# Optimization experiments

Measured on AMD Instinct MI355X. Metric: run time of the kernel, lower is better.

The kernel has to match this reference:

```python
import jax, jax.numpy as jnp
import numpy as np

B, N, D = 16, 1024, 16  # graphs, nodes, embedding_dim


def setup_inputs() -> dict:
    key = jax.random.key(0)
    ks = jax.random.split(key, 13)
    s = 0.05  # small weight scale to keep exp(alpha) well-behaved
    return {
        "X": jax.random.normal(ks[0], (B, N, D), dtype=jnp.float32),
        "init_param": jax.random.normal(ks[1], (2,), dtype=jnp.float32) * s,
        "Wq": jax.random.normal(ks[2], (D - 1, D, D), dtype=jnp.float32) * s,
        "bq": jax.random.normal(ks[3], (D - 1, D), dtype=jnp.float32) * s,
        "Wk": jax.random.normal(ks[4], (D - 1, D, D), dtype=jnp.float32) * s,
        "bk": jax.random.normal(ks[5], (D - 1, D), dtype=jnp.float32) * s,
        "Wv": jax.random.normal(ks[6], (D - 1, D, D), dtype=jnp.float32) * s,
        "bv": jax.random.normal(ks[7], (D - 1, D), dtype=jnp.float32) * s,
        "Wo": jax.random.normal(ks[8], (D - 1, D, D), dtype=jnp.float32) * s,
        "bo": jax.random.normal(ks[9], (D - 1, D), dtype=jnp.float32) * s,
        "Wf": jax.random.normal(ks[10], (D - 1, 2, D), dtype=jnp.float32) * s,
        "bf": jax.random.normal(ks[11], (D - 1, 2), dtype=jnp.float32) * s,
    }


def reference(X, init_param, Wq, bq, Wk, bk, Wv, bv, Wo, bo, Wf, bf):
    b, n, d = X.shape
    dt = X.dtype
    Zs = []
    logdet = jnp.zeros((b, n), dt)
    for i in range(d):
        if i == 0:
            mu, alpha = init_param[0], init_param[1]
        else:
            l = i - 1
            Xi = X[:, :, :i]  # [B,N,i] growing ragged slice
            Q = Xi @ Wq[l, :i, :i].T + bq[l, :i]
            K = Xi @ Wk[l, :i, :i].T + bk[l, :i]
            V = Xi @ Wv[l, :i, :i].T + bv[l, :i]
            # SAB/MAB: softmax(QK^T / sqrt(dim_V=i)); num_heads=1
            A = jax.nn.softmax(
                jnp.einsum("bnd,bmd->bnm", Q, K) / jnp.sqrt(jnp.asarray(i, dt)),
                axis=-1,
            )  # [B,N,N]
            O = Q + jnp.einsum("bnm,bmd->bnd", A, V)
            O = O + jax.nn.relu(O @ Wo[l, :i, :i].T + bo[l, :i])
            out = O @ Wf[l, :, :i].T + bf[l]  # [B,N,2]
            mu, alpha = out[..., 0], out[..., 1]
        Zs.append((X[:, :, i] - mu) / jnp.exp(alpha))
        logdet = logdet - alpha
    Z = jnp.stack(Zs, axis=-1)
    return Z, logdet
```

## Files before the change

kernel.cpp:

```cpp
#include <hip/hip_runtime.h>
#include <math.h>

#define Bb 16
#define Nn 1024
#define Dd 16
#define NL 15

typedef __attribute__((ext_vector_type(8))) short short8;
typedef __attribute__((ext_vector_type(16))) float f32x16;
typedef __attribute__((ext_vector_type(4))) unsigned uint4v;

#if __has_builtin(__builtin_amdgcn_exp2f)
#define EXP2(x) __builtin_amdgcn_exp2f(x)
#else
#define EXP2(x) exp2f(x)
#endif

#define VSTR 1040
#define V_OFF 32768
#define ONES_OFF 66048
#define RS_OFF 69632
#define LDS_TOTAL 73728

__device__ __forceinline__ unsigned pack2bf(float a, float b) {
    unsigned ua = __float_as_uint(a) + 0x8000u;
    unsigned ub = __float_as_uint(b) + 0x8000u;
    return (ua >> 16) | (ub & 0xffff0000u);
}
__device__ __forceinline__ unsigned short bf1(float a) {
    return (unsigned short)((__float_as_uint(a) + 0x8000u) >> 16);
}

__device__ __forceinline__ unsigned expperm(float x, float y) {
    unsigned ex = __float_as_uint(EXP2(x));
    unsigned ey = __float_as_uint(EXP2(y));
#if __has_builtin(__builtin_amdgcn_perm)
    return __builtin_amdgcn_perm(ey, ex, 0x07060302);
#else
    return (ex >> 16) | (ey & 0xffff0000u);
#endif
}

__device__ __forceinline__ int vperm(int m) {
    return (m & 3) + ((m & 8) >> 1) + ((m & 4) << 1);
}

__device__ __forceinline__ void project(const float* __restrict__ xrow,
                                        const float* __restrict__ W,
                                        const float* __restrict__ bias,
                                        int i, float* __restrict__ q) {
#pragma unroll
    for (int r = 0; r < 16; r++) q[r] = 0.f;
    for (int c = 0; c < i; c++) {
        float xc = xrow[c];
#pragma unroll
        for (int r = 0; r < 16; r++) q[r] = fmaf(xc, W[r * 16 + c], q[r]);
    }
#pragma unroll
    for (int r = 0; r < 16; r++) q[r] = (r < i) ? (q[r] + bias[r]) : 0.f;
}

__device__ __forceinline__ void load_row16(const float* __restrict__ p, float* __restrict__ x) {
    const float4* xp = (const float4*)p;
    float4 a = xp[0], b = xp[1], c = xp[2], d = xp[3];
    x[0]=a.x; x[1]=a.y; x[2]=a.z; x[3]=a.w;
    x[4]=b.x; x[5]=b.y; x[6]=b.z; x[7]=b.w;
    x[8]=c.x; x[9]=c.y; x[10]=c.z; x[11]=c.w;
    x[12]=d.x; x[13]=d.y; x[14]=d.z; x[15]=d.w;
}

__global__ void gf_init(const float* __restrict__ X, const float* __restrict__ ip,
                        float* __restrict__ out) {
    int idx = blockIdx.x * blockDim.x + threadIdx.x;
    if (idx >= Bb * Nn) return;
    float mu = ip[0], alpha = ip[1];
    float x0 = X[(size_t)idx * Dd];
    out[(size_t)idx * Dd] = (x0 - mu) * __expf(-alpha);
    out[(size_t)Bb * Nn * Dd + idx] = -alpha;
}

__launch_bounds__(1024, 4)
__global__ void gf_fused(const float* __restrict__ X,
                         const float* __restrict__ Wq, const float* __restrict__ bq,
                         const float* __restrict__ Wk, const float* __restrict__ bk,
                         const float* __restrict__ Wv, const float* __restrict__ bv,
                         const float* __restrict__ Wo, const float* __restrict__ bo,
                         const float* __restrict__ Wf, const float* __restrict__ bf,
                         float* __restrict__ out) {
    extern __shared__ char smem[];
    const int l = blockIdx.x, b = blockIdx.y, i = l + 1;
    const int t = threadIdx.x;
    const int wid = t >> 6, lane = t & 63;
    const int q31 = lane & 31, h = lane >> 5;
    const float qscale = 1.4426950408889634f * rsqrtf((float)i);

    unsigned short* Ksh  = (unsigned short*)smem;
    unsigned short* Vsh  = (unsigned short*)(smem + V_OFF);
    unsigned short* Ones = (unsigned short*)(smem + ONES_OFF);

    const float* Xb  = X  + (size_t)b * Nn * Dd;
    const float* wq  = Wq + l * 256;  const float* bql = bq + l * 16;
    const float* wk  = Wk + l * 256;  const float* bkl = bk + l * 16;
    const float* wvp = Wv + l * 256;  const float* bvl = bv + l * 16;
    const float* wo  = Wo + l * 256;  const float* bol = bo + l * 16;
    const float* wf  = Wf + l * 32;   const float* bfl = bf + l * 2;

    unsigned qu[8];
    {
        float xr[16]; load_row16(Xb + (size_t)t * Dd, xr);
        float tmp[16];

        project(xr, wk, bkl, i, tmp);
        {
            unsigned u[8];
#pragma unroll
            for (int r = 0; r < 8; r++) u[r] = pack2bf(tmp[2*r], tmp[2*r+1]);
            uint4* kd = (uint4*)(Ksh + t * 16);
            kd[0] = make_uint4(u[0], u[1], u[2], u[3]);
            kd[1] = make_uint4(u[4], u[5], u[6], u[7]);
        }

        project(xr, wvp, bvl, i, tmp);
        {
            unsigned short* vcol = Vsh + (t & ~15) + vperm(t & 15);
#pragma unroll
            for (int d = 0; d < 16; d++) vcol[d * VSTR] = bf1(tmp[d]);
        }

        Ones[t] = 0x3F80;

        project(xr, wq, bql, i, tmp);
#pragma unroll
        for (int r = 0; r < 8; r++) qu[r] = pack2bf(tmp[2*r] * qscale, tmp[2*r+1] * qscale);
    }
    __syncthreads();

    short8 qf0, qf1;
    {
        unsigned d0[4], d1[4];
#pragma unroll
        for (int j = 0; j < 4; j++) {
            unsigned lo = __shfl(qu[j], q31);
            unsigned hi = __shfl(qu[4 + j], q31);
            d0[j] = h ? hi : lo;
            lo = __shfl(qu[j], 32 + q31);
            hi = __shfl(qu[4 + j], 32 + q31);
            d1[j] = h ? hi : lo;
        }
        uint4v v0 = {d0[0], d0[1], d0[2], d0[3]};
        uint4v v1 = {d1[0], d1[1], d1[2], d1[3]};
        qf0 = __builtin_bit_cast(short8, v0);
        qf1 = __builtin_bit_cast(short8, v1);
    }

    f32x16 zf16 = {};
    f32x16 D0 = {}, D1 = {};

    const unsigned short* Kp = Ksh + (size_t)q31 * 16 + h * 8;
    const unsigned short* Vp = ((q31 < 16) ? (Vsh + (size_t)q31 * VSTR) : Ones) + 8 * h;

    short8 kf  = *(const short8*)Kp;
    short8 vc0 = *(const short8*)(Vp);
    short8 vc1 = *(const short8*)(Vp + 16);

    for (int kb = 0; kb < Nn; kb += 32) {
        const int kn = (kb + 32) & (Nn - 1);
        short8 kfn = *(const short8*)(Kp + (size_t)kn * 16);
        short8 vn0 = *(const short8*)(Vp + kn);
        short8 vn1 = *(const short8*)(Vp + kn + 16);

        f32x16 s0 = __builtin_amdgcn_mfma_f32_32x32x16_bf16(kf, qf0, zf16, 0, 0, 0);
        f32x16 s1 = __builtin_amdgcn_mfma_f32_32x32x16_bf16(kf, qf1, zf16, 0, 0, 0);
        kf = kfn;

        {
            uint4v a0 = {expperm(s0[0], s0[1]), expperm(s0[2], s0[3]),
                         expperm(s0[4], s0[5]), expperm(s0[6], s0[7])};
            D0 = __builtin_amdgcn_mfma_f32_32x32x16_bf16(
                     __builtin_bit_cast(short8, a0), vc0, D0, 0, 0, 0);
            uint4v a1 = {expperm(s1[0], s1[1]), expperm(s1[2], s1[3]),
                         expperm(s1[4], s1[5]), expperm(s1[6], s1[7])};
            D1 = __builtin_amdgcn_mfma_f32_32x32x16_bf16(
                     __builtin_bit_cast(short8, a1), vc0, D1, 0, 0, 0);
        }
        {
            uint4v a0 = {expperm(s0[8], s0[9]),  expperm(s0[10], s0[11]),
                         expperm(s0[12], s0[13]), expperm(s0[14], s0[15])};
            D0 = __builtin_amdgcn_mfma_f32_32x32x16_bf16(
                     __builtin_bit_cast(short8, a0), vc1, D0, 0, 0, 0);
            uint4v a1 = {expperm(s1[8], s1[9]),  expperm(s1[10], s1[11]),
                         expperm(s1[12], s1[13]), expperm(s1[14], s1[15])};
            D1 = __builtin_amdgcn_mfma_f32_32x32x16_bf16(
                     __builtin_bit_cast(short8, a1), vc1, D1, 0, 0, 0);
        }
        vc0 = vn0; vc1 = vn1;
    }

    __syncthreads();

    float* Ow = (float*)smem + wid * (64 * 17);
    if (q31 < 16) {
#pragma unroll
        for (int r = 0; r < 16; r++) {
            int m = (r & 3) + 8 * (r >> 2) + 4 * h;
            Ow[m * 17 + q31]        = D0[r];
            Ow[(m + 32) * 17 + q31] = D1[r];
        }
    }
    float* Rw = (float*)(smem + RS_OFF) + wid * 64;
    if (q31 == 16) {
#pragma unroll
        for (int r = 0; r < 16; r++) {
            int m = (r & 3) + 8 * (r >> 2) + 4 * h;
            Rw[m]      = D0[r];
            Rw[32 + m] = D1[r];
        }
    }

    {
        const float invq = 0.6931471805599453f * sqrtf((float)i);

        float a[16];
#pragma unroll
        for (int r = 0; r < 8; r++) {
            a[2*r]     = __uint_as_float(qu[r] << 16) * invq;
            a[2*r + 1] = __uint_as_float(qu[r] & 0xffff0000u) * invq;
        }

        const float* orow = (const float*)smem + wid * (64 * 17) + lane * 17;
        const float  inv  = 1.f / Rw[lane];
#pragma unroll
        for (int c = 0; c < 16; c++) a[c] += orow[c] * inv;

        float tt[16];
#pragma unroll
        for (int r = 0; r < 16; r++) {
            float acc = bol[r];
#pragma unroll
            for (int c = 0; c < 16; c++) acc = fmaf(a[c], wo[r * 16 + c], acc);
            tt[r] = fmaxf(acc, 0.f);
        }
#pragma unroll
        for (int r = 0; r < 16; r++) a[r] += (r < i) ? tt[r] : 0.f;

        float mu = bfl[0], al = bfl[1];
#pragma unroll
        for (int c = 0; c < 16; c++) {
            mu = fmaf(a[c], wf[c], mu);
            al = fmaf(a[c], wf[16 + c], al);
        }
        const float xi = Xb[(size_t)t * Dd + i];
        out[((size_t)(b * Nn + t)) * Dd + i] = (xi - mu) * __expf(-al);
        atomicAdd(out + (size_t)Bb * Nn * Dd + b * Nn + t, -al);
    }
}

__launch_bounds__(512, 2)
__global__ void gf_layer_fb(const float* __restrict__ X,
                            const float* __restrict__ Wq, const float* __restrict__ bq,
                            const float* __restrict__ Wk, const float* __restrict__ bk,
                            const float* __restrict__ Wv, const float* __restrict__ bv,
                            const float* __restrict__ Wo, const float* __restrict__ bo,
                            const float* __restrict__ Wf, const float* __restrict__ bf,
                            float* __restrict__ out) {
    const int l = blockIdx.x, b = blockIdx.y, i = l + 1, t = threadIdx.x;
    const float rscale = rsqrtf((float)i);
    __shared__ float Ksh[512 * 16];
    __shared__ float Vsh[512 * 16];
    const float* Xb = X + (size_t)b * Nn * Dd;
    const float* wq = Wq + l * 256; const float* wk = Wk + l * 256;
    const float* wv = Wv + l * 256; const float* wo = Wo + l * 256;
    const float* wf = Wf + l * 32;
    const float* bql = bq + l * 16; const float* bkl = bk + l * 16;
    const float* bvl = bv + l * 16; const float* bol = bo + l * 16;
    const float* bfl = bf + l * 2;
    const int n0 = t, n1 = t + 512;
    float q0[16], q1[16], xi0, xi1;
    {
        float xr[16];
        load_row16(Xb + (size_t)n0 * Dd, xr); xi0 = xr[i]; project(xr, wq, bql, i, q0);
        load_row16(Xb + (size_t)n1 * Dd, xr); xi1 = xr[i]; project(xr, wq, bql, i, q1);
    }
    float o0[16], o1[16];
#pragma unroll
    for (int c = 0; c < 16; c++) { o0[c] = 0.f; o1[c] = 0.f; }
    float ls0 = 0.f, ls1 = 0.f;
    for (int ch = 0; ch < 2; ch++) {
        float kr[16], vr[16];
        {
            float kx[16];
            load_row16(Xb + (size_t)(ch * 512 + t) * Dd, kx);
            project(kx, wk, bkl, i, kr);
            project(kx, wv, bvl, i, vr);
        }
        __syncthreads();
#pragma unroll
        for (int j = 0; j < 4; j++) {
            ((float4*)&Ksh[t * 16])[j] = ((float4*)kr)[j];
            ((float4*)&Vsh[t * 16])[j] = ((float4*)vr)[j];
        }
        __syncthreads();
        for (int k = 0; k < 512; k++) {
            float kk[16], vv[16];
#pragma unroll
            for (int j = 0; j < 4; j++) ((float4*)kk)[j] = ((const float4*)&Ksh[k * 16])[j];
            float s0 = 0.f, s1 = 0.f;
#pragma unroll
            for (int c = 0; c < 16; c++) { s0 = fmaf(q0[c], kk[c], s0); s1 = fmaf(q1[c], kk[c], s1); }
            float p0 = __expf(s0 * rscale), p1 = __expf(s1 * rscale);
            ls0 += p0; ls1 += p1;
#pragma unroll
            for (int j = 0; j < 4; j++) ((float4*)vv)[j] = ((const float4*)&Vsh[k * 16])[j];
#pragma unroll
            for (int c = 0; c < 16; c++) { o0[c] = fmaf(p0, vv[c], o0[c]); o1[c] = fmaf(p1, vv[c], o1[c]); }
        }
        __syncthreads();
    }
    float* logdet = out + (size_t)Bb * Nn * Dd;
#pragma unroll
    for (int rowsel = 0; rowsel < 2; rowsel++) {
        const float* qr = rowsel ? q1 : q0; const float* orr = rowsel ? o1 : o0;
        float lsum = rowsel ? ls1 : ls0; float xin = rowsel ? xi1 : xi0;
        int n = rowsel ? n1 : n0;
        float a[16]; float inv = 1.f / lsum;
#pragma unroll
        for (int c = 0; c < 16; c++) a[c] = qr[c] + orr[c] * inv;
        float tt[16];
#pragma unroll
        for (int r = 0; r < 16; r++) {
            float acc = bol[r];
#pragma unroll
            for (int c = 0; c < 16; c++) acc = fmaf(a[c], wo[r * 16 + c], acc);
            tt[r] = fmaxf(acc, 0.f);
        }
#pragma unroll
        for (int r = 0; r < 16; r++) a[r] += (r < i) ? tt[r] : 0.f;
        float mu = bfl[0], al = bfl[1];
#pragma unroll
        for (int c = 0; c < 16; c++) { mu = fmaf(a[c], wf[c], mu); al = fmaf(a[c], wf[16 + c], al); }
        out[((size_t)(b * Nn + n)) * Dd + i] = (xin - mu) * __expf(-al);
        atomicAdd(logdet + b * Nn + n, -al);
    }
}

extern "C" void kernel_launch(void* const* d_in, const int* in_sizes, int n_in,
                              void* d_out, int out_size, void* d_ws, size_t ws_size,
                              hipStream_t stream) {
    const float* X  = (const float*)d_in[0];
    const float* ip = (const float*)d_in[1];
    const float* Wq = (const float*)d_in[2];
    const float* bq = (const float*)d_in[3];
    const float* Wk = (const float*)d_in[4];
    const float* bk = (const float*)d_in[5];
    const float* Wv = (const float*)d_in[6];
    const float* bv = (const float*)d_in[7];
    const float* Wo = (const float*)d_in[8];
    const float* bo = (const float*)d_in[9];
    const float* Wf = (const float*)d_in[10];
    const float* bf = (const float*)d_in[11];
    float* out = (float*)d_out;

    gf_init<<<(Bb * Nn + 255) / 256, 256, 0, stream>>>(X, ip, out);

    hipError_t e = hipFuncSetAttribute((const void*)gf_fused,
                                       hipFuncAttributeMaxDynamicSharedMemorySize,
                                       LDS_TOTAL);
    if (e == hipSuccess) {
        gf_fused<<<dim3(NL, Bb), 1024, LDS_TOTAL, stream>>>(
            X, Wq, bq, Wk, bk, Wv, bv, Wo, bo, Wf, bf, out);
    } else {
        gf_layer_fb<<<dim3(NL, Bb), 512, 0, stream>>>(
            X, Wq, bq, Wk, bk, Wv, bv, Wo, bo, Wf, bf, out);
    }
}
```

Baseline: 134.5 us.

## Split queries across two blocks and keys across wave halves in fused attention

The grid gains a z dimension of 2, so each block handles 512 query rows instead of 1024. Within a block, waves 0-7 and waves 8-15 each process half of the 1024 keys for the same 512 queries, and the two partial numerators and row sums are combined through LDS before the epilogue. This doubles the block count from 240 to 480 so more of the device's compute units are busy. In exchange, K/V projection and staging is duplicated in both blocks, and an extra barrier plus partial-sum reduction is added.

```diff
diff --git a/kernel.cpp b/kernel.cpp
--- a/kernel.cpp
+++ b/kernel.cpp
@@ -79,7 +79,7 @@
     out[(size_t)Bb * Nn * Dd + idx] = -alpha;
 }
 
-__launch_bounds__(1024, 4)
+__launch_bounds__(1024, 8)
 __global__ void gf_fused(const float* __restrict__ X,
                          const float* __restrict__ Wq, const float* __restrict__ bq,
                          const float* __restrict__ Wk, const float* __restrict__ bk,
@@ -89,9 +89,12 @@
                          float* __restrict__ out) {
     extern __shared__ char smem[];
     const int l = blockIdx.x, b = blockIdx.y, i = l + 1;
+    const int qh = blockIdx.z;
     const int t = threadIdx.x;
     const int wid = t >> 6, lane = t & 63;
     const int q31 = lane & 31, h = lane >> 5;
+    const int kbase = (wid >> 3) << 9;
+    const int qrow = (qh << 9) | (t & 511);
     const float qscale = 1.4426950408889634f * rsqrtf((float)i);
 
     unsigned short* Ksh  = (unsigned short*)smem;
@@ -129,6 +132,8 @@
 
         Ones[t] = 0x3F80;
 
+        if (qrow != t)
+            load_row16(Xb + (size_t)qrow * Dd, xr);
         project(xr, wq, bql, i, tmp);
 #pragma unroll
         for (int r = 0; r < 8; r++) qu[r] = pack2bf(tmp[2*r] * qscale, tmp[2*r+1] * qscale);
@@ -156,15 +161,15 @@
     f32x16 zf16 = {};
     f32x16 D0 = {}, D1 = {};
 
-    const unsigned short* Kp = Ksh + (size_t)q31 * 16 + h * 8;
-    const unsigned short* Vp = ((q31 < 16) ? (Vsh + (size_t)q31 * VSTR) : Ones) + 8 * h;
+    const unsigned short* Kp = Ksh + (size_t)(kbase + q31) * 16 + h * 8;
+    const unsigned short* Vp = ((q31 < 16) ? (Vsh + (size_t)q31 * VSTR) : Ones) + 8 * h + kbase;
 
     short8 kf  = *(const short8*)Kp;
     short8 vc0 = *(const short8*)(Vp);
     short8 vc1 = *(const short8*)(Vp + 16);
 
-    for (int kb = 0; kb < Nn; kb += 32) {
-        const int kn = (kb + 32) & (Nn - 1);
+    for (int lk = 0; lk < 512; lk += 32) {
+        const int kn = (lk + 32) & 511;
         short8 kfn = *(const short8*)(Kp + (size_t)kn * 16);
         short8 vn0 = *(const short8*)(Vp + kn);
         short8 vn1 = *(const short8*)(Vp + kn + 16);
@@ -207,8 +212,9 @@
             Ow[(m + 32) * 17 + q31] = D1[r];
         }
     }
-    float* Rw = (float*)(smem + RS_OFF) + wid * 64;
+    float* Rs = (float*)(smem + RS_OFF);
     if (q31 == 16) {
+        float* Rw = Rs + wid * 64;
 #pragma unroll
         for (int r = 0; r < 16; r++) {
             int m = (r & 3) + 8 * (r >> 2) + 4 * h;
@@ -216,8 +222,9 @@
             Rw[32 + m] = D1[r];
         }
     }
-
-    {
+    __syncthreads();
+
+    if (t < 512) {
         const float invq = 0.6931471805599453f * sqrtf((float)i);
 
         float a[16];
@@ -227,10 +234,12 @@
             a[2*r + 1] = __uint_as_float(qu[r] & 0xffff0000u) * invq;
         }
 
-        const float* orow = (const float*)smem + wid * (64 * 17) + lane * 17;
-        const float  inv  = 1.f / Rw[lane];
-#pragma unroll
-        for (int c = 0; c < 16; c++) a[c] += orow[c] * inv;
+        const float* orow0 = (const float*)smem + wid * (64 * 17) + lane * 17;
+        const float* orow1 = orow0 + 8 * (64 * 17);
+        const float  rsum  = Rs[wid * 64 + lane] + Rs[(wid + 8) * 64 + lane];
+        const float  inv   = 1.f / rsum;
+#pragma unroll
+        for (int c = 0; c < 16; c++) a[c] += (orow0[c] + orow1[c]) * inv;
 
         float tt[16];
 #pragma unroll
@@ -249,9 +258,9 @@
             mu = fmaf(a[c], wf[c], mu);
             al = fmaf(a[c], wf[16 + c], al);
         }
-        const float xi = Xb[(size_t)t * Dd + i];
-        out[((size_t)(b * Nn + t)) * Dd + i] = (xi - mu) * __expf(-al);
-        atomicAdd(out + (size_t)Bb * Nn * Dd + b * Nn + t, -al);
+        const float xi = Xb[(size_t)qrow * Dd + i];
+        out[((size_t)(b * Nn + qrow)) * Dd + i] = (xi - mu) * __expf(-al);
+        atomicAdd(out + (size_t)Bb * Nn * Dd + b * Nn + qrow, -al);
     }
 }
 
@@ -366,7 +375,7 @@
                                        hipFuncAttributeMaxDynamicSharedMemorySize,
                                        LDS_TOTAL);
     if (e == hipSuccess) {
-        gf_fused<<<dim3(NL, Bb), 1024, LDS_TOTAL, stream>>>(
+        gf_fused<<<dim3(NL, Bb, 2), 1024, LDS_TOTAL, stream>>>(
             X, Wq, bq, Wk, bk, Wv, bv, Wo, bo, Wf, bf, out);
     } else {
         gf_layer_fb<<<dim3(NL, Bb), 512, 0, stream>>>(
```

New measurement: 497.9 us. +270.1%, slower.

## Split fused layer kernel into projection and query-tiled attention kernels

Applied to the files above, without the earlier changes.

Moves the Q/K/V projections into a separate kernel that writes bf16 Q, K and a permuted V to workspace. A second kernel then splits each (layer, batch) attention problem into 8 query tiles across 1920 blocks of 256 threads instead of 240 blocks of 1024 threads. K and V stream from global memory rather than LDS, and a ones vector stands in for the row sums. This is meant to raise occupancy and balance work across CUs, at the cost of an extra launch and an extra round trip of projections through global memory. The logdet is accumulated with atomicAdd.

```diff
diff --git a/kernel.cpp b/kernel.cpp
--- a/kernel.cpp
+++ b/kernel.cpp
@@ -15,6 +15,9 @@
 #else
 #define EXP2(x) exp2f(x)
 #endif
+
+#define PROJ_SZ ((size_t)NL * Bb * 1024 * 16)
+#define WS_NEED (3 * PROJ_SZ * 2 + 1088 * 2)
 
 #define VSTR 1040
 #define V_OFF 32768
@@ -70,13 +73,187 @@
 }
 
 __global__ void gf_init(const float* __restrict__ X, const float* __restrict__ ip,
-                        float* __restrict__ out) {
+                        float* __restrict__ out, unsigned short* __restrict__ onesb) {
     int idx = blockIdx.x * blockDim.x + threadIdx.x;
     if (idx >= Bb * Nn) return;
+    if (onesb && idx < 1088) onesb[idx] = 0x3F80;
     float mu = ip[0], alpha = ip[1];
     float x0 = X[(size_t)idx * Dd];
     out[(size_t)idx * Dd] = (x0 - mu) * __expf(-alpha);
     out[(size_t)Bb * Nn * Dd + idx] = -alpha;
+}
+
+__global__ void gf_proj(const float* __restrict__ X,
+                        const float* __restrict__ Wq, const float* __restrict__ bq,
+                        const float* __restrict__ Wk, const float* __restrict__ bk,
+                        const float* __restrict__ Wv, const float* __restrict__ bv,
+                        unsigned short* __restrict__ Kg,
+                        unsigned short* __restrict__ Vg,
+                        unsigned short* __restrict__ Qg) {
+    const int l = blockIdx.x, b = blockIdx.y, i = l + 1;
+    const int t = threadIdx.x;
+    const size_t lb = (size_t)(l * Bb + b);
+    const float qscale = 1.4426950408889634f * rsqrtf((float)i);
+
+    const float* Xb  = X  + (size_t)b * Nn * Dd;
+    const float* wq  = Wq + l * 256;  const float* bql = bq + l * 16;
+    const float* wk  = Wk + l * 256;  const float* bkl = bk + l * 16;
+    const float* wvp = Wv + l * 256;  const float* bvl = bv + l * 16;
+
+    float xr[16]; load_row16(Xb + (size_t)t * Dd, xr);
+    float tmp[16];
+
+    project(xr, wk, bkl, i, tmp);
+    {
+        unsigned u[8];
+#pragma unroll
+        for (int r = 0; r < 8; r++) u[r] = pack2bf(tmp[2*r], tmp[2*r+1]);
+        uint4* kd = (uint4*)(Kg + (lb * 1024 + t) * 16);
+        kd[0] = make_uint4(u[0], u[1], u[2], u[3]);
+        kd[1] = make_uint4(u[4], u[5], u[6], u[7]);
+    }
+
+    project(xr, wvp, bvl, i, tmp);
+    {
+        unsigned short* vcol = Vg + lb * (16 * 1024) + (t & ~15) + vperm(t & 15);
+#pragma unroll
+        for (int d = 0; d < 16; d++) vcol[d * 1024] = bf1(tmp[d]);
+    }
+
+    project(xr, wq, bql, i, tmp);
+    {
+        unsigned u[8];
+#pragma unroll
+        for (int r = 0; r < 8; r++) u[r] = pack2bf(tmp[2*r] * qscale, tmp[2*r+1] * qscale);
+        uint4* qd = (uint4*)(Qg + (lb * 1024 + t) * 16);
+        qd[0] = make_uint4(u[0], u[1], u[2], u[3]);
+        qd[1] = make_uint4(u[4], u[5], u[6], u[7]);
+    }
+}
+
+__launch_bounds__(256, 5)
+__global__ void gf_attn(const float* __restrict__ X,
+                        const unsigned short* __restrict__ Kg,
+                        const unsigned short* __restrict__ Vg,
+                        const unsigned short* __restrict__ Qg,
+                        const unsigned short* __restrict__ onesb,
+                        const float* __restrict__ Wo, const float* __restrict__ bo,
+                        const float* __restrict__ Wf, const float* __restrict__ bf,
+                        float* __restrict__ out) {
+    __shared__ float Osh[4 * 32 * 17];
+    __shared__ float Rsh[4 * 32];
+
+    const int bx = blockIdx.x;
+    const int c = bx & 7, k = bx >> 3;
+    const int G = c * 30 + (k >> 3);
+    const int z = k & 7;
+    const int l = G % NL, b = G / NL, i = l + 1;
+
+    const int t = threadIdx.x;
+    const int wid = t >> 6, lane = t & 63;
+    const int q31 = lane & 31, h = lane >> 5;
+    const size_t lb = (size_t)(l * Bb + b);
+    const int qbase = z * 128 + wid * 32;
+
+    short8 qf = *(const short8*)(Qg + (lb * 1024 + qbase + q31) * 16 + 8 * h);
+
+    const unsigned short* Kp = Kg + (lb * 1024 + q31) * 16 + 8 * h;
+    const unsigned short* Vp = ((q31 < 16) ? (Vg + (lb * 16 + q31) * 1024)
+                                           : onesb) + 8 * h;
+
+    const f32x16 zf16 = {};
+    f32x16 D = {};
+
+    short8 kf  = *(const short8*)Kp;
+    short8 vc0 = *(const short8*)(Vp);
+    short8 vc1 = *(const short8*)(Vp + 16);
+
+    for (int lk = 0; lk < Nn; lk += 32) {
+        const int kn = (lk + 32) & (Nn - 1);
+        short8 kfn = *(const short8*)(Kp + (size_t)kn * 16);
+        short8 vn0 = *(const short8*)(Vp + kn);
+        short8 vn1 = *(const short8*)(Vp + kn + 16);
+
+        f32x16 s = __builtin_amdgcn_mfma_f32_32x32x16_bf16(kf, qf, zf16, 0, 0, 0);
+
+        {
+            uint4v a0 = {expperm(s[0], s[1]), expperm(s[2], s[3]),
+                         expperm(s[4], s[5]), expperm(s[6], s[7])};
+            D = __builtin_amdgcn_mfma_f32_32x32x16_bf16(
+                    __builtin_bit_cast(short8, a0), vc0, D, 0, 0, 0);
+        }
+        {
+            uint4v a1 = {expperm(s[8], s[9]),  expperm(s[10], s[11]),
+                         expperm(s[12], s[13]), expperm(s[14], s[15])};
+            D = __builtin_amdgcn_mfma_f32_32x32x16_bf16(
+                    __builtin_bit_cast(short8, a1), vc1, D, 0, 0, 0);
+        }
+        kf = kfn; vc0 = vn0; vc1 = vn1;
+    }
+
+    float* Ow = Osh + wid * (32 * 17);
+    if (q31 < 16) {
+#pragma unroll
+        for (int r = 0; r < 16; r++) {
+            int m = (r & 3) + 8 * (r >> 2) + 4 * h;
+            Ow[m * 17 + q31] = D[r];
+        }
+    }
+    if (q31 == 16) {
+        float* Rw = Rsh + wid * 32;
+#pragma unroll
+        for (int r = 0; r < 16; r++) {
+            int m = (r & 3) + 8 * (r >> 2) + 4 * h;
+            Rw[m] = D[r];
+        }
+    }
+    __syncthreads();
+
+    if (t < 128) {
+        const int qn = z * 128 + t;
+        const float invq = 0.6931471805599453f * sqrtf((float)i);
+
+        float a[16];
+        {
+            const uint4* qp = (const uint4*)(Qg + (lb * 1024 + qn) * 16);
+            uint4 u0 = qp[0], u1 = qp[1];
+            unsigned uw[8] = {u0.x, u0.y, u0.z, u0.w, u1.x, u1.y, u1.z, u1.w};
+#pragma unroll
+            for (int r = 0; r < 8; r++) {
+                a[2*r]     = __uint_as_float(uw[r] << 16) * invq;
+                a[2*r + 1] = __uint_as_float(uw[r] & 0xffff0000u) * invq;
+            }
+        }
+
+        const float* orow = Osh + (t >> 5) * (32 * 17) + (t & 31) * 17;
+        const float  inv  = 1.f / Rsh[(t >> 5) * 32 + (t & 31)];
+#pragma unroll
+        for (int cc = 0; cc < 16; cc++) a[cc] += orow[cc] * inv;
+
+        const float* wo  = Wo + l * 256;  const float* bol = bo + l * 16;
+        const float* wf  = Wf + l * 32;   const float* bfl = bf + l * 2;
+
+        float tt[16];
+#pragma unroll
+        for (int r = 0; r < 16; r++) {
+            float acc = bol[r];
+#pragma unroll
+            for (int cc = 0; cc < 16; cc++) acc = fmaf(a[cc], wo[r * 16 + cc], acc);
+            tt[r] = fmaxf(acc, 0.f);
+        }
+#pragma unroll
+        for (int r = 0; r < 16; r++) a[r] += (r < i) ? tt[r] : 0.f;
+
+        float mu = bfl[0], al = bfl[1];
+#pragma unroll
+        for (int cc = 0; cc < 16; cc++) {
+            mu = fmaf(a[cc], wf[cc], mu);
+            al = fmaf(a[cc], wf[16 + cc], al);
+        }
+        const float xi = X[((size_t)b * Nn + qn) * Dd + i];
+        out[((size_t)(b * Nn + qn)) * Dd + i] = (xi - mu) * __expf(-al);
+        atomicAdd(out + (size_t)Bb * Nn * Dd + b * Nn + qn, -al);
+    }
 }
 
 __launch_bounds__(1024, 4)
@@ -360,7 +537,21 @@
     const float* bf = (const float*)d_in[11];
     float* out = (float*)d_out;
 
-    gf_init<<<(Bb * Nn + 255) / 256, 256, 0, stream>>>(X, ip, out);
+    if (ws_size >= WS_NEED && d_ws != nullptr) {
+        unsigned short* Kg    = (unsigned short*)d_ws;
+        unsigned short* Vg    = Kg + PROJ_SZ;
+        unsigned short* Qg    = Vg + PROJ_SZ;
+        unsigned short* onesb = Qg + PROJ_SZ;
+
+        gf_init<<<(Bb * Nn + 255) / 256, 256, 0, stream>>>(X, ip, out, onesb);
+        gf_proj<<<dim3(NL, Bb), 1024, 0, stream>>>(X, Wq, bq, Wk, bk, Wv, bv,
+                                                   Kg, Vg, Qg);
+        gf_attn<<<NL * Bb * 8, 256, 0, stream>>>(X, Kg, Vg, Qg, onesb,
+                                                 Wo, bo, Wf, bf, out);
+        return;
+    }
+
+    gf_init<<<(Bb * Nn + 255) / 256, 256, 0, stream>>>(X, ip, out, nullptr);
 
     hipError_t e = hipFuncSetAttribute((const void*)gf_fused,
                                        hipFuncAttributeMaxDynamicSharedMemorySize,
```

New measurement: 166.3 us. 1.24x slower.
